# Kernel tuning notes

Measured on AMD Instinct MI355X. Metric: run time of the kernel, lower is better.

The kernel has to match this reference:

```python
import jax, jax.numpy as jnp
import numpy as np

B, S, D, H = 2, 4096, 1024, 16
DH = D // H            # head dim = 64
W = 256                # one-sided attention window (attention_window // 2)
NC = S // W            # number of query chunks
NEG = -1e9


def setup_inputs() -> dict:
    key = jax.random.key(0)
    ks = jax.random.split(key, 8)
    sc = 0.02
    return {
        "hidden_states": jax.random.normal(ks[0], (B, S, D), jnp.float32),
        # additive float mask: 0 = local token, <0 = padding, >0 = global. All zeros here.
        "attention_mask": jnp.zeros((B, 1, 1, S), jnp.float32),
        "Wq": jax.random.normal(ks[1], (D, D), jnp.float32) * sc,
        "bq": jnp.zeros((D,), jnp.float32),
        "Wk": jax.random.normal(ks[2], (D, D), jnp.float32) * sc,
        "bk": jnp.zeros((D,), jnp.float32),
        "Wv": jax.random.normal(ks[3], (D, D), jnp.float32) * sc,
        "bv": jnp.zeros((D,), jnp.float32),
        "Wo": jax.random.normal(ks[4], (D, D), jnp.float32) * sc,
        "bo": jnp.zeros((D,), jnp.float32),
    }


def _heads(x, w, b):
    # [B,S,D] -> [B,H,S,DH]
    return (x @ w + b).reshape(B, S, H, DH).transpose(0, 2, 1, 3)


def _forward(hidden_states, attention_mask, Wq, bq, Wk, bk, Wv, bv, Wo, bo):
    mask = attention_mask[:, 0, 0, :]                    # [B,S] additive key mask
    q = _heads(hidden_states, Wq, bq) / jnp.sqrt(jnp.float32(DH))
    k = _heads(hidden_states, Wk, bk)
    v = _heads(hidden_states, Wv, bv)

    # Overlapping key/value chunks: chunk c covers padded positions [c*W, c*W+3W),
    # i.e. global keys [c*W - W, c*W + 2W) -- the union of the windows of its W queries.
    idx = jnp.arange(NC)[:, None] * W + jnp.arange(3 * W)[None, :]   # [NC,3W] into padded axis
    k_pad = jnp.pad(k, ((0, 0), (0, 0), (W, W), (0, 0)))
    v_pad = jnp.pad(v, ((0, 0), (0, 0), (W, W), (0, 0)))
    k_ch = k_pad[:, :, idx]                               # [B,H,NC,3W,DH]
    v_ch = v_pad[:, :, idx]                               # [B,H,NC,3W,DH]
    mask_ch = jnp.pad(mask, ((0, 0), (W, W)))[:, idx]     # [B,NC,3W]

    q_ch = q.reshape(B, H, NC, W, DH)
    scores = jnp.einsum('bhcqd,bhckd->bhcqk', q_ch, k_ch)  # [B,H,NC,W,3W]

    # Band mask: query local p attends key local o with 0 <= o - p <= 2W.
    rel = jnp.arange(3 * W)[None, :] - jnp.arange(W)[:, None]        # [W,3W]
    band = (rel >= 0) & (rel <= 2 * W)
    key_gidx = idx - W                                               # global key index
    valid = (key_gidx >= 0) & (key_gidx < S)                         # [NC,3W]
    allowed = band[None, :, :] & valid[:, None, :]                   # [NC,W,3W]

    scores = scores + mask_ch[:, None, :, None, :]
    scores = jnp.where(allowed[None, None], scores, NEG)
    probs = jax.nn.softmax(scores, axis=-1)

    out = jnp.einsum('bhcqk,bhckd->bhcqd', probs, v_ch)    # [B,H,NC,W,DH]
    out = out.reshape(B, H, S, DH).transpose(0, 2, 1, 3).reshape(B, S, D)
    return out @ Wo + bo


def reference(hidden_states, attention_mask, Wq, bq, Wk, bk, Wv, bv, Wo, bo):
    return _forward(hidden_states, attention_mask, Wq, bq, Wk, bk, Wv, bv, Wo, bo)
```

## Files before the change

### kernel.cpp

```cpp
#include <hip/hip_runtime.h>

typedef unsigned short u16;
typedef __bf16 bf16x8 __attribute__((ext_vector_type(8)));
typedef u16 u16x8 __attribute__((ext_vector_type(8)));
typedef float f32x4 __attribute__((ext_vector_type(4)));
typedef unsigned uint2v __attribute__((ext_vector_type(2)));

#define LOG2E 1.4426950408889634f

static __device__ __forceinline__ u16 f2bf(float f) {
    union { float f; unsigned u; } x; x.f = f;
    unsigned r = x.u + 0x7fffu + ((x.u >> 16) & 1u);
    return (u16)(r >> 16);
}

static __device__ __forceinline__ unsigned cvtpk(float lo, float hi) {
    unsigned r;
    asm("v_cvt_pk_bf16_f32 %0, %1, %2" : "=v"(r) : "v"(lo), "v"(hi));
    return r;
}

static __device__ __forceinline__ void gl_lds16(const void* g, void* l) {
    __builtin_amdgcn_global_load_lds(
        (const __attribute__((address_space(1))) void*)g,
        (__attribute__((address_space(3))) void*)l, 16, 0, 0);
}

__global__ __launch_bounds__(256) void cvt_k(const float* __restrict__ src,
                                             u16* __restrict__ dst, int n) {
    int i = (blockIdx.x * 256 + threadIdx.x) * 4;
    if (i < n) {
        float4 v = *(const float4*)(src + i);
        ushort4 o;
        o.x = f2bf(v.x); o.y = f2bf(v.y); o.z = f2bf(v.z); o.w = f2bf(v.w);
        *(ushort4*)(dst + i) = o;
    }
}

__global__ __launch_bounds__(256) void transw_k(const float* __restrict__ w0,
                                                const float* __restrict__ w1,
                                                const float* __restrict__ w2,
                                                const float* __restrict__ w3,
                                                u16* __restrict__ wt) {
    __shared__ float T[64][65];
    const float* src = (blockIdx.z == 0) ? w0 : (blockIdx.z == 1) ? w1
                     : (blockIdx.z == 2) ? w2 : w3;
    u16* dst = wt + (size_t)blockIdx.z * 1048576;
    const int k0 = blockIdx.x * 64, n0 = blockIdx.y * 64;
    const int rr = threadIdx.x >> 6, col = threadIdx.x & 63;
#pragma unroll
    for (int i = 0; i < 16; ++i) {
        int row = i * 4 + rr;
        T[row][col] = src[(size_t)(k0 + row) * 1024 + n0 + col];
    }
    __syncthreads();
#pragma unroll
    for (int i = 0; i < 16; ++i) {
        int row = i * 4 + rr;
        dst[(size_t)(n0 + row) * 1024 + k0 + col] = f2bf(T[col][row]);
    }
}

template<int MODE>
__global__ __launch_bounds__(256) void gemm_t(
    const u16* __restrict__ A, const u16* __restrict__ WT0,
    const float* __restrict__ b0, const float* __restrict__ b1,
    u16* __restrict__ o0, u16* __restrict__ o1, float* __restrict__ oF) {
    __shared__ alignas(16) u16 Al[128 * 32];
    __shared__ alignas(16) u16 Bl[128 * 32];

    const int tid = threadIdx.x;
    const int lane = tid & 63;
    const int wv = tid >> 6;
    const int wr = wv >> 1, wc = wv & 1;
    const int l15 = lane & 15, l4 = lane >> 4;

    const int mbase = blockIdx.x * 128;
    const int sel = (MODE == 0) ? (blockIdx.y >> 3) : 0;
    const int nb = (blockIdx.y & 7) * 128;

    const u16* Ab = A + (size_t)mbase * 1024;
    const u16* Bb = WT0 + (size_t)sel * 1048576 + (size_t)nb * 1024;

    const int srow = tid >> 2;
    const int scol = (tid & 3) * 8;

    f32x4 acc[4][4] = {};

    for (int k0 = 0; k0 < 1024; k0 += 32) {
        char* la = (char*)Al + wv * 1024;
        char* lb = (char*)Bl + wv * 1024;
        gl_lds16(Ab + (size_t)srow * 1024 + k0 + scol, la);
        gl_lds16(Ab + (size_t)(srow + 64) * 1024 + k0 + scol, la + 4096);
        gl_lds16(Bb + (size_t)srow * 1024 + k0 + scol, lb);
        gl_lds16(Bb + (size_t)(srow + 64) * 1024 + k0 + scol, lb + 4096);
        __syncthreads();

        bf16x8 af[4], bfr[4];
#pragma unroll
        for (int mr = 0; mr < 4; ++mr)
            af[mr] = *(const bf16x8*)(Al + (wr * 64 + mr * 16 + l15) * 32 + l4 * 8);
#pragma unroll
        for (int nr = 0; nr < 4; ++nr)
            bfr[nr] = *(const bf16x8*)(Bl + (wc * 64 + nr * 16 + l15) * 32 + l4 * 8);
        if constexpr (MODE == 2) {
#pragma unroll
            for (int mr = 0; mr < 4; ++mr)
#pragma unroll
                for (int nr = 0; nr < 4; ++nr)
                    acc[mr][nr] = __builtin_amdgcn_mfma_f32_16x16x32_bf16(
                        bfr[nr], af[mr], acc[mr][nr], 0, 0, 0);
        } else {
#pragma unroll
            for (int mr = 0; mr < 4; ++mr)
#pragma unroll
                for (int nr = 0; nr < 4; ++nr)
                    acc[mr][nr] = __builtin_amdgcn_mfma_f32_16x16x32_bf16(
                        af[mr], bfr[nr], acc[mr][nr], 0, 0, 0);
        }
        __syncthreads();
    }

    if constexpr (MODE == 2) {
#pragma unroll
        for (int mr = 0; mr < 4; ++mr) {
            int srow2 = mbase + wr * 64 + mr * 16 + l15;
            int b_ = srow2 >> 12, s_ = srow2 & 4095;
#pragma unroll
            for (int nr = 0; nr < 4; ++nr) {
                f32x4 bvv = *(const f32x4*)(b0 + nb + wc * 64 + nr * 16 + l4 * 4);
#pragma unroll
                for (int j = 0; j < 4; ++j) {
                    int c2 = nb + wc * 64 + nr * 16 + l4 * 4 + j;
                    float v = acc[mr][nr][j] + bvv[j];
                    o0[(((size_t)(b_ * 16 + (c2 >> 6)) * 64 + (c2 & 63)) * 4096) + s_] = f2bf(v);
                }
            }
        }
        return;
    }

    const float* bias = (MODE == 0 && sel == 1) ? b1 : b0;
    u16* oH = (sel == 0) ? o0 : o1;
    const float scale = (MODE == 0 && sel == 0) ? 0.125f * LOG2E : 1.0f;

#pragma unroll
    for (int mr = 0; mr < 4; ++mr)
#pragma unroll
        for (int nr = 0; nr < 4; ++nr) {
            int col = nb + wc * 64 + nr * 16 + l15;
            float bv_ = bias[col];
#pragma unroll
            for (int j = 0; j < 4; ++j) {
                int row = mbase + wr * 64 + mr * 16 + l4 * 4 + j;
                float v = (acc[mr][nr][j] + bv_) * scale;
                if constexpr (MODE == 0) {
                    int b_ = row >> 12, s_ = row & 4095;
                    int h_ = col >> 6, d_ = col & 63;
                    oH[(((size_t)(b_ * 16 + h_) * 4096) + s_) * 64 + d_] = f2bf(v);
                } else {
                    oF[(size_t)row * 1024 + col] = v;
                }
            }
        }
}

__global__ __launch_bounds__(256) void attn_k(
    const u16* __restrict__ Qh, const u16* __restrict__ Kh,
    const u16* __restrict__ Vt, const float* __restrict__ mask,
    u16* __restrict__ attnb) {
    __shared__ alignas(16) u16 VtL[2][4096];
    __shared__ alignas(16) u16 Pl[4][1024];
    __shared__ alignas(16) float maskl[640];

    const int tid = threadIdx.x;
    const int lane = tid & 63;
    const int wv = tid >> 6;
    const int hw = blockIdx.x;
    const int lg = (hw & 7) * 128 + (hw >> 3);
    const int c = lg & 31;
    const int h = (lg >> 5) & 15;
    const int b = lg >> 9;

    const size_t bh = (size_t)(b * 16 + h) * 4096;
    const u16* Qb = Qh + bh * 64;
    const u16* Kb = Kh + bh * 64;
    const u16* Vb = Vt + bh * 64;
    const float* mb = mask + b * 4096;

    const int l15 = lane & 15;
    const int l4 = lane >> 4;
    const int qbase = c * 128 + wv * 32;
    const int gkbase = c * 128 - 256;

    bf16x8 qf[2][2];
#pragma unroll
    for (int qt = 0; qt < 2; ++qt)
#pragma unroll
        for (int kc = 0; kc < 2; ++kc)
            qf[qt][kc] = *(const bf16x8*)(Qb + (size_t)(qbase + qt * 16 + l15) * 64 + kc * 32 + l4 * 8);

    f32x4 Ov[4][2] = {};
    float lsum[2] = {0.f, 0.f};
    float m[2] = {-3.0e38f, -3.0e38f};

    auto stageV = [&](int buf, int gk) {
#pragma unroll
        for (int i = 0; i < 2; ++i) {
            int d = i * 32 + wv * 8 + (lane >> 3);
            int s = lane & 7;
            int col = min(max(gk + ((s ^ (d & 7)) * 8), 0), 4088);
            gl_lds16(Vb + (size_t)d * 4096 + col, &VtL[buf][(i * 32 + wv * 8) * 64]);
        }
    };

    stageV(0, gkbase);
    for (int i = tid; i < 640; i += 256) {
        int gm = gkbase + i;
        maskl[i] = (gm >= 0 && gm < 4096) ? mb[gm] * LOG2E : 0.f;
    }
    __syncthreads();

    const int tmin = wv >> 1;
    const int tmaxw = 8 + (wv >> 1);

    for (int t = 0; t < 10; ++t) {
        const int cur = t & 1, nxt = cur ^ 1;
        const int gk0 = gkbase + t * 64;
        if (t < 9) stageV(nxt, gk0 + 64);

        if (t >= tmin && t <= tmaxw) {
            bf16x8 kfr[2][4];
#pragma unroll
            for (int kc = 0; kc < 2; ++kc)
#pragma unroll
                for (int kb = 0; kb < 4; ++kb) {
                    int key = min(max(gk0 + kb * 16 + l15, 0), 4095);
                    kfr[kc][kb] = *(const bf16x8*)(Kb + (size_t)key * 64 + kc * 32 + l4 * 8);
                }

            f32x4 mv[4];
#pragma unroll
            for (int kb = 0; kb < 4; ++kb)
                mv[kb] = *(const f32x4*)(maskl + t * 64 + kb * 16 + l4 * 4);

            f32x4 sc[4][2] = {};
            __builtin_amdgcn_s_setprio(1);
#pragma unroll
            for (int kc = 0; kc < 2; ++kc)
#pragma unroll
                for (int kb = 0; kb < 4; ++kb) {
                    sc[kb][0] = __builtin_amdgcn_mfma_f32_16x16x32_bf16(kfr[kc][kb], qf[0][kc], sc[kb][0], 0, 0, 0);
                    sc[kb][1] = __builtin_amdgcn_mfma_f32_16x16x32_bf16(kfr[kc][kb], qf[1][kc], sc[kb][1], 0, 0, 0);
                }
            __builtin_amdgcn_s_setprio(0);

            const int dkq = gk0 - qbase;
            const bool full = (dkq >= -225) && (dkq <= 193) && (gk0 >= 0) && (gk0 <= 4032);
            if (full) {
#pragma unroll
                for (int kb = 0; kb < 4; ++kb)
#pragma unroll
                    for (int qt = 0; qt < 2; ++qt)
#pragma unroll
                        for (int j = 0; j < 4; ++j)
                            sc[kb][qt][j] += mv[kb][j];
            } else {
                const int kb0 = gk0 + l4 * 4;
                const int ub0 = kb0 - (qbase + l15) + 256;
#pragma unroll
                for (int kb = 0; kb < 4; ++kb)
#pragma unroll
                    for (int qt = 0; qt < 2; ++qt)
#pragma unroll
                        for (int j = 0; j < 4; ++j) {
                            float sv = sc[kb][qt][j] + mv[kb][j];
                            unsigned band = (unsigned)(ub0 + kb * 16 + j - qt * 16);
                            unsigned keyv = (unsigned)(kb0 + kb * 16 + j);
                            bool ok = (band <= 512u) && (keyv < 4096u);
                            sc[kb][qt][j] = ok ? sv : -3.0e9f;
                        }
            }

            u16* Pw = &Pl[wv][0];
            const int prow = l15 * 64;
#pragma unroll
            for (int qt = 0; qt < 2; ++qt) {
                float mx = sc[0][qt][0];
#pragma unroll
                for (int kb = 0; kb < 4; ++kb)
#pragma unroll
                    for (int j = 0; j < 4; ++j) mx = fmaxf(mx, sc[kb][qt][j]);
                mx = fmaxf(mx, __shfl_xor(mx, 16));
                mx = fmaxf(mx, __shfl_xor(mx, 32));
                float mnew = fmaxf(m[qt], mx);
                float alpha = exp2f(m[qt] - mnew);
                m[qt] = mnew;
                lsum[qt] *= alpha;
#pragma unroll
                for (int nd = 0; nd < 4; ++nd) Ov[nd][qt] *= alpha;

                float s0 = 0.f;
#pragma unroll
                for (int kb = 0; kb < 4; ++kb) {
                    float p0 = exp2f(sc[kb][qt][0] - mnew);
                    float p1 = exp2f(sc[kb][qt][1] - mnew);
                    float p2 = exp2f(sc[kb][qt][2] - mnew);
                    float p3 = exp2f(sc[kb][qt][3] - mnew);
                    s0 += (p0 + p1) + (p2 + p3);
                    uint2v pk;
                    pk[0] = cvtpk(p0, p1);
                    pk[1] = cvtpk(p2, p3);
                    int g = (((kb * 2 + (l4 >> 1)) ^ (l15 & 7)) * 8) + (l4 & 1) * 4;
                    *(uint2v*)(Pw + prow + g) = pk;
                }
                lsum[qt] += s0;

#pragma unroll
                for (int kc = 0; kc < 2; ++kc) {
                    bf16x8 pf = *(const bf16x8*)(Pw + prow + (((kc * 4 + l4) ^ (l15 & 7)) * 8));
                    __builtin_amdgcn_s_setprio(1);
#pragma unroll
                    for (int nd = 0; nd < 4; ++nd) {
                        int r2 = nd * 16 + l15;
                        bf16x8 vf = *(const bf16x8*)(&VtL[cur][r2 * 64 +
                            (((kc * 4 + l4) ^ (r2 & 7)) * 8)]);
                        Ov[nd][qt] = __builtin_amdgcn_mfma_f32_16x16x32_bf16(vf, pf, Ov[nd][qt], 0, 0, 0);
                    }
                    __builtin_amdgcn_s_setprio(0);
                }
            }
        }
        __syncthreads();
    }

    lsum[0] += __shfl_xor(lsum[0], 16);
    lsum[0] += __shfl_xor(lsum[0], 32);
    lsum[1] += __shfl_xor(lsum[1], 16);
    lsum[1] += __shfl_xor(lsum[1], 32);
    float inv0 = 1.0f / lsum[0];
    float inv1 = 1.0f / lsum[1];
#pragma unroll
    for (int qt = 0; qt < 2; ++qt) {
        float inv = qt ? inv1 : inv0;
        size_t rowb = ((size_t)b * 4096 + qbase + qt * 16 + l15) * 1024 + h * 64 + l4 * 4;
#pragma unroll
        for (int nd = 0; nd < 4; ++nd) {
            uint2v o;
            o[0] = cvtpk(Ov[nd][qt][0] * inv, Ov[nd][qt][1] * inv);
            o[1] = cvtpk(Ov[nd][qt][2] * inv, Ov[nd][qt][3] * inv);
            *(uint2v*)(&attnb[rowb + nd * 16]) = o;
        }
    }
}

extern "C" void kernel_launch(void* const* d_in, const int* in_sizes, int n_in,
                              void* d_out, int out_size, void* d_ws, size_t ws_size,
                              hipStream_t stream) {
    (void)in_sizes; (void)n_in; (void)out_size; (void)ws_size;
    const float* hid  = (const float*)d_in[0];
    const float* mask = (const float*)d_in[1];
    const float* Wq = (const float*)d_in[2];
    const float* bq = (const float*)d_in[3];
    const float* Wk = (const float*)d_in[4];
    const float* bk = (const float*)d_in[5];
    const float* Wv = (const float*)d_in[6];
    const float* bv = (const float*)d_in[7];
    const float* Wo = (const float*)d_in[8];
    const float* bo = (const float*)d_in[9];
    float* out = (float*)d_out;

    char* ws = (char*)d_ws;
    u16* hidb  = (u16*)(ws);
    u16* wt    = (u16*)(ws + (16u << 20));
    u16* Qh    = (u16*)(ws + (24u << 20));
    u16* Kh    = (u16*)(ws + (40u << 20));
    u16* Vtb   = (u16*)(ws + (56u << 20));
    u16* attnb = (u16*)(ws + (72u << 20));

    cvt_k<<<dim3(8192), dim3(256), 0, stream>>>(hid, hidb, 8388608);
    transw_k<<<dim3(16, 16, 4), dim3(256), 0, stream>>>(Wq, Wk, Wv, Wo, wt);
    gemm_t<0><<<dim3(64, 16), dim3(256), 0, stream>>>(hidb, wt, bq, bk,
                                                      Qh, Kh, (float*)nullptr);
    gemm_t<2><<<dim3(64, 8), dim3(256), 0, stream>>>(hidb, wt + 2 * 1048576, bv, (const float*)nullptr,
                                                     Vtb, (u16*)nullptr, (float*)nullptr);
    attn_k<<<dim3(1024), dim3(256), 0, stream>>>(Qh, Kh, Vtb, mask, attnb);
    gemm_t<1><<<dim3(64, 8), dim3(256), 0, stream>>>(attnb, wt + 3 * 1048576, bo, (const float*)nullptr,
                                                     (u16*)nullptr, (u16*)nullptr, out);
}
```

Measured before the change: 188.4 us.

## Stage K tiles through double-buffered LDS and skip softmax rescale when max stable

K tiles are now loaded into a double-buffered, swizzled LDS array alongside V with async global-to-LDS copies. The score MFMAs read K fragments from LDS instead of doing direct global loads inside the loop, so K fetch latency is meant to overlap with the previous tile's compute. Separately, the online-softmax max update and the rescaling of the output accumulator are skipped when every lane's tile max stays within a threshold of the running max (a lazy rescale). This adds 16KB of LDS per block, which may lower occupancy, and lets exp2 arguments reach up to about +8. That is bounded and safe in fp32 but changes the rounding in the bf16 probabilities.

```diff
diff --git a/kernel.cpp b/kernel.cpp
--- a/kernel.cpp
+++ b/kernel.cpp
@@ -169,6 +169,7 @@
     const u16* __restrict__ Qh, const u16* __restrict__ Kh,
     const u16* __restrict__ Vt, const float* __restrict__ mask,
     u16* __restrict__ attnb) {
+    __shared__ alignas(16) u16 Kt[2][4096];
     __shared__ alignas(16) u16 VtL[2][4096];
     __shared__ alignas(16) u16 Pl[4][1024];
     __shared__ alignas(16) float maskl[640];
@@ -204,6 +205,16 @@
     float lsum[2] = {0.f, 0.f};
     float m[2] = {-3.0e38f, -3.0e38f};
 
+    auto stageK = [&](int buf, int gk) {
+#pragma unroll
+        for (int i = 0; i < 2; ++i) {
+            int r = i * 32 + wv * 8 + (lane >> 3);
+            int s = lane & 7;
+            int key = min(max(gk + r, 0), 4095);
+            gl_lds16(Kb + (size_t)key * 64 + ((s ^ (r & 7)) * 8),
+                     &Kt[buf][(i * 32 + wv * 8) * 64]);
+        }
+    };
     auto stageV = [&](int buf, int gk) {
 #pragma unroll
         for (int i = 0; i < 2; ++i) {
@@ -214,6 +225,7 @@
         }
     };
 
+    stageK(0, gkbase);
     stageV(0, gkbase);
     for (int i = tid; i < 640; i += 256) {
         int gm = gkbase + i;
@@ -227,18 +239,9 @@
     for (int t = 0; t < 10; ++t) {
         const int cur = t & 1, nxt = cur ^ 1;
         const int gk0 = gkbase + t * 64;
-        if (t < 9) stageV(nxt, gk0 + 64);
+        if (t < 9) { stageK(nxt, gk0 + 64); stageV(nxt, gk0 + 64); }
 
         if (t >= tmin && t <= tmaxw) {
-            bf16x8 kfr[2][4];
-#pragma unroll
-            for (int kc = 0; kc < 2; ++kc)
-#pragma unroll
-                for (int kb = 0; kb < 4; ++kb) {
-                    int key = min(max(gk0 + kb * 16 + l15, 0), 4095);
-                    kfr[kc][kb] = *(const bf16x8*)(Kb + (size_t)key * 64 + kc * 32 + l4 * 8);
-                }
-
             f32x4 mv[4];
 #pragma unroll
             for (int kb = 0; kb < 4; ++kb)
@@ -250,8 +253,10 @@
             for (int kc = 0; kc < 2; ++kc)
 #pragma unroll
                 for (int kb = 0; kb < 4; ++kb) {
-                    sc[kb][0] = __builtin_amdgcn_mfma_f32_16x16x32_bf16(kfr[kc][kb], qf[0][kc], sc[kb][0], 0, 0, 0);
-                    sc[kb][1] = __builtin_amdgcn_mfma_f32_16x16x32_bf16(kfr[kc][kb], qf[1][kc], sc[kb][1], 0, 0, 0);
+                    int r = kb * 16 + l15;
+                    bf16x8 kf = *(const bf16x8*)(&Kt[cur][r * 64 + (((kc * 4 + l4) ^ (r & 7)) * 8)]);
+                    sc[kb][0] = __builtin_amdgcn_mfma_f32_16x16x32_bf16(kf, qf[0][kc], sc[kb][0], 0, 0, 0);
+                    sc[kb][1] = __builtin_amdgcn_mfma_f32_16x16x32_bf16(kf, qf[1][kc], sc[kb][1], 0, 0, 0);
                 }
             __builtin_amdgcn_s_setprio(0);
 
@@ -291,22 +296,24 @@
                 for (int kb = 0; kb < 4; ++kb)
 #pragma unroll
                     for (int j = 0; j < 4; ++j) mx = fmaxf(mx, sc[kb][qt][j]);
-                mx = fmaxf(mx, __shfl_xor(mx, 16));
-                mx = fmaxf(mx, __shfl_xor(mx, 32));
-                float mnew = fmaxf(m[qt], mx);
-                float alpha = exp2f(m[qt] - mnew);
-                m[qt] = mnew;
-                lsum[qt] *= alpha;
-#pragma unroll
-                for (int nd = 0; nd < 4; ++nd) Ov[nd][qt] *= alpha;
+                if (!__all(mx <= m[qt] + 8.0f)) {
+                    mx = fmaxf(mx, __shfl_xor(mx, 16));
+                    mx = fmaxf(mx, __shfl_xor(mx, 32));
+                    float mnew = fmaxf(m[qt], mx);
+                    float alpha = exp2f(m[qt] - mnew);
+                    m[qt] = mnew;
+                    lsum[qt] *= alpha;
+#pragma unroll
+                    for (int nd = 0; nd < 4; ++nd) Ov[nd][qt] *= alpha;
+                }
 
                 float s0 = 0.f;
 #pragma unroll
                 for (int kb = 0; kb < 4; ++kb) {
-                    float p0 = exp2f(sc[kb][qt][0] - mnew);
-                    float p1 = exp2f(sc[kb][qt][1] - mnew);
-                    float p2 = exp2f(sc[kb][qt][2] - mnew);
-                    float p3 = exp2f(sc[kb][qt][3] - mnew);
+                    float p0 = exp2f(sc[kb][qt][0] - m[qt]);
+                    float p1 = exp2f(sc[kb][qt][1] - m[qt]);
+                    float p2 = exp2f(sc[kb][qt][2] - m[qt]);
+                    float p3 = exp2f(sc[kb][qt][3] - m[qt]);
                     s0 += (p0 + p1) + (p2 + p3);
                     uint2v pk;
                     pk[0] = cvtpk(p0, p1);
```

New measurement: 174.4 us. 7.4% less time.
